# Performance work log

Measured on AMD Instinct MI355X. Metric: run time of the kernel, lower is better.

## Reference

```python
import jax, jax.numpy as jnp
import numpy as np

ALPHA = 0.2  # LeakyReLU negative slope
NEG_INF = -9e15


def setup_inputs() -> dict:
    key = jax.random.key(0)
    ks = jax.random.split(key, 6)
    N, IN, OUT, E = 2048, 256, 256, 64
    inp = {
        "input": jax.random.normal(ks[0], (N, IN), dtype=jnp.float32),
        "adj": jax.random.randint(ks[1], (N, N), 0, 2, dtype=jnp.int32),
        "e_feat": jax.random.normal(ks[2], (N, N, E), dtype=jnp.float32),
        # xavier-uniform-like scale for params
        "W_e": jax.random.normal(ks[3], (E, IN), dtype=jnp.float32) * (1.414 * np.sqrt(2.0 / (E + IN))),
        "W": jax.random.normal(ks[4], (IN, OUT), dtype=jnp.float32) * (1.414 * np.sqrt(2.0 / (IN + OUT))),
        "a": jax.random.normal(ks[5], (3 * OUT, 1), dtype=jnp.float32) * (1.414 * np.sqrt(2.0 / (3 * OUT + 1))),
    }
    return inp


def reference(input, adj, e_feat, W_e, W, a):
    F = W.shape[1]
    # Decompose attention vector: cat([h_i, h_j, e_ij]) @ a == h_i@a1 + h_j@a2 + e_ij@a3
    a1, a2, a3 = a[:F, 0], a[F:2 * F, 0], a[2 * F:, 0]
    h = input @ W                              # [N, F]
    s_src = h @ a1                             # [N]
    s_dst = h @ a2                             # [N]
    # e_ij @ a3 where e = e_feat @ W_e @ W, folded by associativity into one [N,N] result
    s_edge = e_feat @ (W_e @ (W @ a3))         # [N, N]
    scores = jax.nn.leaky_relu(s_src[:, None] + s_dst[None, :] + s_edge, negative_slope=ALPHA)
    att = jnp.where(adj > 0, scores, NEG_INF)
    att = jax.nn.softmax(att, axis=1)
    h_prime = att @ h                          # [N, F]
    return jax.nn.elu(h_prime)                 # concat=True -> ELU
```

## Files before the change

### kernel.cpp

```cpp
#include <hip/hip_runtime.h>
#include <math.h>

#define NN   2048
#define INF_ 256
#define OUTF 256
#define EF   64
#define ALPHA 0.2f
#define NEG_INF -9000000000000000.0f

typedef unsigned short ushortT;
typedef __attribute__((ext_vector_type(8))) short    short8v;
typedef __attribute__((ext_vector_type(4))) short    short4v;
typedef __attribute__((ext_vector_type(8))) unsigned short u16x8;
typedef __attribute__((ext_vector_type(4))) float    f32x4;
typedef __attribute__((ext_vector_type(4))) float    fv4;
typedef __attribute__((ext_vector_type(4))) int      iv4;

__device__ __forceinline__ ushortT f2b(float f) {
    unsigned b = *(unsigned*)&f;
    unsigned r = (b + 0x7FFFu + ((b >> 16) & 1u)) >> 16;
    return (ushortT)r;
}
__device__ __forceinline__ float dpp_add_xor1(float x) {
    int xi = *(int*)&x;
    int r = __builtin_amdgcn_mov_dpp(xi, 0xB1, 0xF, 0xF, true);
    float rf = *(float*)&r;
    return x + rf;
}
__device__ __forceinline__ float dpp_add_xor2(float x) {
    int xi = *(int*)&x;
    int r = __builtin_amdgcn_mov_dpp(xi, 0x4E, 0xF, 0xF, true);
    float rf = *(float*)&r;
    return x + rf;
}
__device__ __forceinline__ fv4 ntload4(const float* p) {
    return __builtin_nontemporal_load((const fv4*)p);
}

__global__ void prep1_kernel(const float* __restrict__ W, const float* __restrict__ a,
                             float* __restrict__ w3) {
    int lane = threadIdx.x & 63, wave = threadIdx.x >> 6;
    const float* a3 = a + 2 * OUTF;
    float4 av = *(const float4*)&a3[lane * 4];
    int r0 = blockIdx.x * 8 + wave * 2;
    #pragma unroll
    for (int rr = 0; rr < 2; ++rr) {
        int r = r0 + rr;
        float4 wv = *(const float4*)&W[(size_t)r * OUTF + lane * 4];
        float d = wv.x * av.x + wv.y * av.y + wv.z * av.z + wv.w * av.w;
        #pragma unroll
        for (int off = 32; off; off >>= 1) d += __shfl_xor(d, off);
        if (lane == 0) w3[r] = d;
    }
}

__global__ void prep2_kernel(const float* __restrict__ W_e, const float* __restrict__ w3,
                             float* __restrict__ we3) {
    int lane = threadIdx.x & 63, wave = threadIdx.x >> 6;
    int r = blockIdx.x * 4 + wave;
    float4 wv = *(const float4*)&W_e[(size_t)r * INF_ + lane * 4];
    float4 xv = *(const float4*)&w3[lane * 4];
    float d = wv.x * xv.x + wv.y * xv.y + wv.z * xv.z + wv.w * xv.w;
    #pragma unroll
    for (int off = 32; off; off >>= 1) d += __shfl_xor(d, off);
    if (lane == 0) we3[r] = d;
}

template<int K>
__launch_bounds__(256, 2)
__global__ void gemm_kernel(const float* __restrict__ A, const float* __restrict__ Bm,
                            float* __restrict__ C) {
    __shared__ float As[64][68];
    __shared__ float Bs[64][32];
    int tid = threadIdx.x;
    int r0 = blockIdx.x * 64;
    int c0 = blockIdx.y * 32;
    int tr = tid >> 4;
    int tc = tid & 15;
    float acc[4][2] = {};

    for (int k0 = 0; k0 < K; k0 += 64) {
        #pragma unroll
        for (int t = 0; t < 4; ++t) {
            int s = tid + t * 256;
            int row = s >> 4, col4 = s & 15;
            *(float4*)&As[row][col4 * 4] =
                *(const float4*)&A[(size_t)(r0 + row) * K + k0 + col4 * 4];
        }
        #pragma unroll
        for (int t = 0; t < 2; ++t) {
            int s = tid + t * 256;
            int row = s >> 3, col4 = s & 7;
            *(float4*)&Bs[row][col4 * 4] =
                *(const float4*)&Bm[(size_t)(k0 + row) * 256 + c0 + col4 * 4];
        }
        __syncthreads();
        #pragma unroll
        for (int kk = 0; kk < 64; kk += 4) {
            float4 aReg[4];
            float2 bReg[4];
            #pragma unroll
            for (int i = 0; i < 4; ++i) aReg[i] = *(const float4*)&As[tr * 4 + i][kk];
            #pragma unroll
            for (int q = 0; q < 4; ++q)  bReg[q] = *(const float2*)&Bs[kk + q][tc * 2];
            #pragma unroll
            for (int q = 0; q < 4; ++q) {
                float bx = bReg[q].x, by = bReg[q].y;
                #pragma unroll
                for (int i = 0; i < 4; ++i) {
                    float av = (q == 0) ? aReg[i].x : (q == 1) ? aReg[i].y
                             : (q == 2) ? aReg[i].z : aReg[i].w;
                    acc[i][0] += av * bx;
                    acc[i][1] += av * by;
                }
            }
        }
        __syncthreads();
    }
    #pragma unroll
    for (int i = 0; i < 4; ++i) {
        int r = r0 + tr * 4 + i;
        float2 v = {acc[i][0], acc[i][1]};
        *(float2*)&C[(size_t)r * 256 + c0 + tc * 2] = v;
    }
}

__global__ void xpose_sv_kernel(const float* __restrict__ h, const float* __restrict__ a,
                                ushortT* __restrict__ hbT,
                                float* __restrict__ s_src, float* __restrict__ s_dst) {
    __shared__ ushortT tb[64][72];
    int b = blockIdx.x;
    int t = threadIdx.x;
    if (b < 128) {
        int r0 = (b >> 2) * 64;
        int n0 = (b & 3) * 64;
        int row = t >> 2, seg = t & 3;
        #pragma unroll
        for (int c = 0; c < 4; ++c) {
            float4 v = *(const float4*)&h[(size_t)(r0 + row) * OUTF + n0 + seg * 16 + c * 4];
            tb[seg * 16 + c * 4 + 0][row] = f2b(v.x);
            tb[seg * 16 + c * 4 + 1][row] = f2b(v.y);
            tb[seg * 16 + c * 4 + 2][row] = f2b(v.z);
            tb[seg * 16 + c * 4 + 3][row] = f2b(v.w);
        }
        __syncthreads();
        *(u16x8*)&hbT[(size_t)(n0 + row) * NN + r0 + seg * 16] =
            *(const u16x8*)&tb[row][seg * 16];
        *(u16x8*)&hbT[(size_t)(n0 + row) * NN + r0 + seg * 16 + 8] =
            *(const u16x8*)&tb[row][seg * 16 + 8];
    } else {
        int lane = t & 63;
        int wave = t >> 6;
        int i = (b - 128) * 4 + wave;
        float acc1 = 0.f, acc2 = 0.f;
        #pragma unroll
        for (int u = 0; u < 4; ++u) {
            int o = lane + u * 64;
            float hv = h[(size_t)i * OUTF + o];
            acc1 += hv * a[o];
            acc2 += hv * a[OUTF + o];
        }
        #pragma unroll
        for (int off = 32; off; off >>= 1) {
            acc1 += __shfl_xor(acc1, off);
            acc2 += __shfl_xor(acc2, off);
        }
        if (lane == 0) { s_src[i] = acc1; s_dst[i] = acc2; }
    }
}

__launch_bounds__(256, 2)
__global__ void gemm2_mfma_kernel(const ushortT* __restrict__ attb,
                                  const ushortT* __restrict__ hbT,
                                  float* __restrict__ Cpart) {
    __shared__ ushortT As[64][72];
    __shared__ ushortT Bs[64][72];
    int tid = threadIdx.x;
    int lane = tid & 63;
    int w = tid >> 6;
    int r0 = blockIdx.x * 64;
    int c0 = blockIdx.y * 64;
    int z  = blockIdx.z;
    int m = lane & 15, q = lane >> 4;
    const int srow = tid >> 2, sseg = tid & 3;

    f32x4 acc0 = {0.f, 0.f, 0.f, 0.f};
    f32x4 acc1 = {0.f, 0.f, 0.f, 0.f};
    f32x4 acc2 = {0.f, 0.f, 0.f, 0.f};
    f32x4 acc3 = {0.f, 0.f, 0.f, 0.f};

    for (int k0 = z * (NN / 4); k0 < (z + 1) * (NN / 4); k0 += 64) {
        {
            const size_t abase = (size_t)(r0 + srow) * NN + k0 + sseg * 16;
            *(u16x8*)&As[srow][sseg * 16]     = *(const u16x8*)&attb[abase];
            *(u16x8*)&As[srow][sseg * 16 + 8] = *(const u16x8*)&attb[abase + 8];
            const size_t bbase = (size_t)(c0 + srow) * NN + k0 + sseg * 16;
            *(u16x8*)&Bs[srow][sseg * 16]     = *(const u16x8*)&hbT[bbase];
            *(u16x8*)&Bs[srow][sseg * 16 + 8] = *(const u16x8*)&hbT[bbase + 8];
        }
        __syncthreads();
        #pragma unroll
        for (int kk = 0; kk < 2; ++kk) {
            short4v a0 = *(const short4v*)&As[w * 16 + m][kk * 32 + q * 4];
            short4v a1 = *(const short4v*)&As[w * 16 + m][kk * 32 + 16 + q * 4];
            short8v af = {a0.x, a0.y, a0.z, a0.w, a1.x, a1.y, a1.z, a1.w};
            #pragma unroll
            for (int nb = 0; nb < 4; ++nb) {
                short4v b0 = *(const short4v*)&Bs[nb * 16 + m][kk * 32 + q * 4];
                short4v b1 = *(const short4v*)&Bs[nb * 16 + m][kk * 32 + 16 + q * 4];
                short8v bf = {b0.x, b0.y, b0.z, b0.w, b1.x, b1.y, b1.z, b1.w};
                if (nb == 0) acc0 = __builtin_amdgcn_mfma_f32_16x16x32_bf16(af, bf, acc0, 0, 0, 0);
                if (nb == 1) acc1 = __builtin_amdgcn_mfma_f32_16x16x32_bf16(af, bf, acc1, 0, 0, 0);
                if (nb == 2) acc2 = __builtin_amdgcn_mfma_f32_16x16x32_bf16(af, bf, acc2, 0, 0, 0);
                if (nb == 3) acc3 = __builtin_amdgcn_mfma_f32_16x16x32_bf16(af, bf, acc3, 0, 0, 0);
            }
        }
        __syncthreads();
    }
    float* Cz = Cpart + (size_t)z * NN * OUTF;
    #pragma unroll
    for (int r = 0; r < 4; ++r) {
        int row = r0 + w * 16 + q * 4 + r;
        Cz[(size_t)row * OUTF + c0 + 0  + m] = acc0[r];
        Cz[(size_t)row * OUTF + c0 + 16 + m] = acc1[r];
        Cz[(size_t)row * OUTF + c0 + 32 + m] = acc2[r];
        Cz[(size_t)row * OUTF + c0 + 48 + m] = acc3[r];
    }
}

__global__ void combine_kernel(const float* __restrict__ Cpart, const float* __restrict__ invs,
                               float* __restrict__ out) {
    int i = blockIdx.x, t = threadIdx.x;
    size_t idx = (size_t)i * OUTF + t;
    const size_t P = (size_t)NN * OUTF;
    float v = (Cpart[idx] + Cpart[P + idx] + Cpart[2 * P + idx] + Cpart[3 * P + idx]) * invs[i];
    out[idx] = v > 0.f ? v : __expf(v) - 1.f;
}

__launch_bounds__(256, 6)
__global__ void score_kernel(const float* __restrict__ e_feat, const int* __restrict__ adj,
                             const float* __restrict__ s_src, const float* __restrict__ s_dst,
                             const float* __restrict__ we3,
                             ushortT* __restrict__ attb, float* __restrict__ invs) {
    __shared__ float p[NN];
    __shared__ float sdst[NN];
    __shared__ unsigned char amask[NN];
    __shared__ float swe3[EF];
    __shared__ float redm[4], reds[4];

    int tid  = threadIdx.x;
    int lane = tid & 63;
    int wave = tid >> 6;
    int i    = blockIdx.x;

    const int* arow = adj + (size_t)i * NN;
    #pragma unroll
    for (int t = 0; t < 2; ++t) {
        int s = tid * 2 + t;
        iv4 a4 = __builtin_nontemporal_load(&((const iv4*)arow)[s]);
        uchar4 m4;
        m4.x = a4.x != 0; m4.y = a4.y != 0; m4.z = a4.z != 0; m4.w = a4.w != 0;
        *(uchar4*)&amask[s * 4] = m4;
        ((float4*)sdst)[s] = ((const float4*)s_dst)[s];
    }
    if (tid < EF) swe3[tid] = we3[tid];
    __syncthreads();

    const int g  = lane >> 2;
    const int gl = lane & 3;
    const float4 wv0 = *(const float4*)&swe3[0  + gl * 4];
    const float4 wv1 = *(const float4*)&swe3[16 + gl * 4];
    const float4 wv2 = *(const float4*)&swe3[32 + gl * 4];
    const float4 wv3 = *(const float4*)&swe3[48 + gl * 4];
    const float* efrow = e_feat + (size_t)i * NN * EF;
    const int joff = wave * 16 + g;

    unsigned mbits = 0;
    #pragma unroll
    for (int k = 0; k < 32; ++k)
        mbits |= (unsigned)(amask[k * 64 + joff] != 0) << k;

    #pragma unroll 4
    for (int k = 0; k < 32; ++k) {
        int j = k * 64 + joff;
        bool av = (mbits >> k) & 1u;
        fv4 e0, e1, e2, e3;
        if (av) {
            const float* ep = efrow + (size_t)j * EF;
            e0 = ntload4(&ep[0  + gl * 4]);
            e1 = ntload4(&ep[16 + gl * 4]);
            e2 = ntload4(&ep[32 + gl * 4]);
            e3 = ntload4(&ep[48 + gl * 4]);
        }
        if (av) {
            float d = e0.x * wv0.x + e0.y * wv0.y + e0.z * wv0.z + e0.w * wv0.w
                    + e1.x * wv1.x + e1.y * wv1.y + e1.z * wv1.z + e1.w * wv1.w
                    + e2.x * wv2.x + e2.y * wv2.y + e2.z * wv2.z + e2.w * wv2.w
                    + e3.x * wv3.x + e3.y * wv3.y + e3.z * wv3.z + e3.w * wv3.w;
            d = dpp_add_xor1(d);
            d = dpp_add_xor2(d);
            if (gl == 0) p[j] = d;
        }
    }
    __syncthreads();

    const float ssrc = s_src[i];

    float m = NEG_INF;
    for (int j = tid; j < NN; j += 256) {
        if (amask[j]) {
            float s = ssrc + sdst[j] + p[j];
            s = (s > 0.f) ? s : ALPHA * s;
            m = fmaxf(m, s);
        }
    }
    #pragma unroll
    for (int off = 32; off; off >>= 1) m = fmaxf(m, __shfl_xor(m, off));
    if (lane == 0) redm[wave] = m;
    __syncthreads();
    m = fmaxf(fmaxf(redm[0], redm[1]), fmaxf(redm[2], redm[3]));
    const bool none = (m < -8.0e14f);

    ushortT* arowo = attb + (size_t)i * NN;
    float sum = 0.f;
    for (int j = tid * 2; j < NN; j += 512) {
        float e0, e1;
        if (amask[j]) {
            float s = ssrc + sdst[j] + p[j];
            s = (s > 0.f) ? s : ALPHA * s;
            e0 = __expf(s - m);
        } else e0 = none ? 1.0f : 0.0f;
        if (amask[j + 1]) {
            float s = ssrc + sdst[j + 1] + p[j + 1];
            s = (s > 0.f) ? s : ALPHA * s;
            e1 = __expf(s - m);
        } else e1 = none ? 1.0f : 0.0f;
        ushort2 uu; uu.x = f2b(e0); uu.y = f2b(e1);
        *(ushort2*)&arowo[j] = uu;
        sum += e0 + e1;
    }
    #pragma unroll
    for (int off = 32; off; off >>= 1) sum += __shfl_xor(sum, off);
    if (lane == 0) reds[wave] = sum;
    __syncthreads();
    if (tid == 0) invs[i] = 1.f / (reds[0] + reds[1] + reds[2] + reds[3]);
}

extern "C" void kernel_launch(void* const* d_in, const int* in_sizes, int n_in,
                              void* d_out, int out_size, void* d_ws, size_t ws_size,
                              hipStream_t stream) {
    const float* input  = (const float*)d_in[0];
    const int*   adj    = (const int*)  d_in[1];
    const float* e_feat = (const float*)d_in[2];
    const float* W_e    = (const float*)d_in[3];
    const float* W      = (const float*)d_in[4];
    const float* a      = (const float*)d_in[5];
    float* out = (float*)d_out;

    float*   ws    = (float*)d_ws;
    float*   h     = ws;
    float*   s_src = h + (size_t)NN * OUTF;
    float*   s_dst = s_src + NN;
    float*   w3    = s_dst + NN;
    float*   we3   = w3 + INF_;
    float*   invs  = we3 + EF;
    ushortT* attb  = (ushortT*)(invs + NN);
    ushortT* hbT   = attb + (size_t)NN * NN;
    float*   cpart = (float*)(hbT + (size_t)OUTF * NN);

    prep1_kernel<<<32, 256, 0, stream>>>(W, a, w3);
    prep2_kernel<<<16, 256, 0, stream>>>(W_e, w3, we3);
    gemm_kernel<INF_><<<dim3(NN / 64, 8), 256, 0, stream>>>(input, W, h);
    xpose_sv_kernel<<<128 + NN / 4, 256, 0, stream>>>(h, a, hbT, s_src, s_dst);
    score_kernel<<<NN, 256, 0, stream>>>(e_feat, adj, s_src, s_dst, we3, attb, invs);
    gemm2_mfma_kernel<<<dim3(NN / 64, OUTF / 64, 4), 256, 0, stream>>>(attb, hbT, cpart);
    combine_kernel<<<NN, 256, 0, stream>>>(cpart, invs, out);
}
```

Baseline: 141.6 us.

## Fold attention vectors into W and merge h GEMM into score mega-kernel

```diff
diff --git a/kernel.cpp b/kernel.cpp
--- a/kernel.cpp
+++ b/kernel.cpp
@@ -37,128 +37,55 @@
     return __builtin_nontemporal_load((const fv4*)p);
 }
 
-__global__ void prep1_kernel(const float* __restrict__ W, const float* __restrict__ a,
-                             float* __restrict__ w3) {
+__global__ void prep_w_kernel(const float* __restrict__ W, const float* __restrict__ a,
+                              float* __restrict__ wa1, float* __restrict__ wa2,
+                              float* __restrict__ w3) {
     int lane = threadIdx.x & 63, wave = threadIdx.x >> 6;
-    const float* a3 = a + 2 * OUTF;
-    float4 av = *(const float4*)&a3[lane * 4];
+    float4 a1v = *(const float4*)&a[lane * 4];
+    float4 a2v = *(const float4*)&a[OUTF + lane * 4];
+    float4 a3v = *(const float4*)&a[2 * OUTF + lane * 4];
     int r0 = blockIdx.x * 8 + wave * 2;
     #pragma unroll
     for (int rr = 0; rr < 2; ++rr) {
         int r = r0 + rr;
         float4 wv = *(const float4*)&W[(size_t)r * OUTF + lane * 4];
-        float d = wv.x * av.x + wv.y * av.y + wv.z * av.z + wv.w * av.w;
+        float d1 = wv.x * a1v.x + wv.y * a1v.y + wv.z * a1v.z + wv.w * a1v.w;
+        float d2 = wv.x * a2v.x + wv.y * a2v.y + wv.z * a2v.z + wv.w * a2v.w;
+        float d3 = wv.x * a3v.x + wv.y * a3v.y + wv.z * a3v.z + wv.w * a3v.w;
+        #pragma unroll
+        for (int off = 32; off; off >>= 1) {
+            d1 += __shfl_xor(d1, off);
+            d2 += __shfl_xor(d2, off);
+            d3 += __shfl_xor(d3, off);
+        }
+        if (lane == 0) { wa1[r] = d1; wa2[r] = d2; w3[r] = d3; }
+    }
+}
+
+__global__ void prep2_sv2_kernel(const float* __restrict__ W_e, const float* __restrict__ w3,
+                                 const float* __restrict__ input,
+                                 const float* __restrict__ wa1, const float* __restrict__ wa2,
+                                 float* __restrict__ we3,
+                                 float* __restrict__ s_src, float* __restrict__ s_dst) {
+    int b = blockIdx.x, t = threadIdx.x;
+    int lane = t & 63, wave = t >> 6;
+    if (b < 16) {
+        int r = b * 4 + wave;
+        float4 wv = *(const float4*)&W_e[(size_t)r * INF_ + lane * 4];
+        float4 xv = *(const float4*)&w3[lane * 4];
+        float d = wv.x * xv.x + wv.y * xv.y + wv.z * xv.z + wv.w * xv.w;
         #pragma unroll
         for (int off = 32; off; off >>= 1) d += __shfl_xor(d, off);
-        if (lane == 0) w3[r] = d;
-    }
-}
-
-__global__ void prep2_kernel(const float* __restrict__ W_e, const float* __restrict__ w3,
-                             float* __restrict__ we3) {
-    int lane = threadIdx.x & 63, wave = threadIdx.x >> 6;
-    int r = blockIdx.x * 4 + wave;
-    float4 wv = *(const float4*)&W_e[(size_t)r * INF_ + lane * 4];
-    float4 xv = *(const float4*)&w3[lane * 4];
-    float d = wv.x * xv.x + wv.y * xv.y + wv.z * xv.z + wv.w * xv.w;
-    #pragma unroll
-    for (int off = 32; off; off >>= 1) d += __shfl_xor(d, off);
-    if (lane == 0) we3[r] = d;
-}
-
-template<int K>
-__launch_bounds__(256, 2)
-__global__ void gemm_kernel(const float* __restrict__ A, const float* __restrict__ Bm,
-                            float* __restrict__ C) {
-    __shared__ float As[64][68];
-    __shared__ float Bs[64][32];
-    int tid = threadIdx.x;
-    int r0 = blockIdx.x * 64;
-    int c0 = blockIdx.y * 32;
-    int tr = tid >> 4;
-    int tc = tid & 15;
-    float acc[4][2] = {};
-
-    for (int k0 = 0; k0 < K; k0 += 64) {
-        #pragma unroll
-        for (int t = 0; t < 4; ++t) {
-            int s = tid + t * 256;
-            int row = s >> 4, col4 = s & 15;
-            *(float4*)&As[row][col4 * 4] =
-                *(const float4*)&A[(size_t)(r0 + row) * K + k0 + col4 * 4];
-        }
-        #pragma unroll
-        for (int t = 0; t < 2; ++t) {
-            int s = tid + t * 256;
-            int row = s >> 3, col4 = s & 7;
-            *(float4*)&Bs[row][col4 * 4] =
-                *(const float4*)&Bm[(size_t)(k0 + row) * 256 + c0 + col4 * 4];
-        }
-        __syncthreads();
-        #pragma unroll
-        for (int kk = 0; kk < 64; kk += 4) {
-            float4 aReg[4];
-            float2 bReg[4];
-            #pragma unroll
-            for (int i = 0; i < 4; ++i) aReg[i] = *(const float4*)&As[tr * 4 + i][kk];
-            #pragma unroll
-            for (int q = 0; q < 4; ++q)  bReg[q] = *(const float2*)&Bs[kk + q][tc * 2];
-            #pragma unroll
-            for (int q = 0; q < 4; ++q) {
-                float bx = bReg[q].x, by = bReg[q].y;
-                #pragma unroll
-                for (int i = 0; i < 4; ++i) {
-                    float av = (q == 0) ? aReg[i].x : (q == 1) ? aReg[i].y
-                             : (q == 2) ? aReg[i].z : aReg[i].w;
-                    acc[i][0] += av * bx;
-                    acc[i][1] += av * by;
-                }
-            }
-        }
-        __syncthreads();
-    }
-    #pragma unroll
-    for (int i = 0; i < 4; ++i) {
-        int r = r0 + tr * 4 + i;
-        float2 v = {acc[i][0], acc[i][1]};
-        *(float2*)&C[(size_t)r * 256 + c0 + tc * 2] = v;
-    }
-}
-
-__global__ void xpose_sv_kernel(const float* __restrict__ h, const float* __restrict__ a,
-                                ushortT* __restrict__ hbT,
-                                float* __restrict__ s_src, float* __restrict__ s_dst) {
-    __shared__ ushortT tb[64][72];
-    int b = blockIdx.x;
-    int t = threadIdx.x;
-    if (b < 128) {
-        int r0 = (b >> 2) * 64;
-        int n0 = (b & 3) * 64;
-        int row = t >> 2, seg = t & 3;
-        #pragma unroll
-        for (int c = 0; c < 4; ++c) {
-            float4 v = *(const float4*)&h[(size_t)(r0 + row) * OUTF + n0 + seg * 16 + c * 4];
-            tb[seg * 16 + c * 4 + 0][row] = f2b(v.x);
-            tb[seg * 16 + c * 4 + 1][row] = f2b(v.y);
-            tb[seg * 16 + c * 4 + 2][row] = f2b(v.z);
-            tb[seg * 16 + c * 4 + 3][row] = f2b(v.w);
-        }
-        __syncthreads();
-        *(u16x8*)&hbT[(size_t)(n0 + row) * NN + r0 + seg * 16] =
-            *(const u16x8*)&tb[row][seg * 16];
-        *(u16x8*)&hbT[(size_t)(n0 + row) * NN + r0 + seg * 16 + 8] =
-            *(const u16x8*)&tb[row][seg * 16 + 8];
+        if (lane == 0) we3[r] = d;
     } else {
-        int lane = t & 63;
-        int wave = t >> 6;
-        int i = (b - 128) * 4 + wave;
+        int i = (b - 16) * 4 + wave;
         float acc1 = 0.f, acc2 = 0.f;
         #pragma unroll
         for (int u = 0; u < 4; ++u) {
             int o = lane + u * 64;
-            float hv = h[(size_t)i * OUTF + o];
-            acc1 += hv * a[o];
-            acc2 += hv * a[OUTF + o];
+            float iv = input[(size_t)i * INF_ + o];
+            acc1 += iv * wa1[o];
+            acc2 += iv * wa2[o];
         }
         #pragma unroll
         for (int off = 32; off; off >>= 1) {
@@ -169,89 +96,98 @@
     }
 }
 
-__launch_bounds__(256, 2)
-__global__ void gemm2_mfma_kernel(const ushortT* __restrict__ attb,
-                                  const ushortT* __restrict__ hbT,
-                                  float* __restrict__ Cpart) {
-    __shared__ ushortT As[64][72];
-    __shared__ ushortT Bs[64][72];
+struct ScSmem {
+    float p[NN];
+    float sdst[NN];
+    unsigned char amask[NN];
+    float swe3[EF];
+    float redm[4], reds[4];
+};
+struct GmSmem {
+    float As[64][68];
+    float Bs[64][32];
+};
+union MegaSmem { ScSmem sc; GmSmem gm; };
+
+__launch_bounds__(256, 6)
+__global__ void mega_kernel(const float* __restrict__ input, const float* __restrict__ W,
+                            const float* __restrict__ e_feat, const int* __restrict__ adj,
+                            const float* __restrict__ s_src, const float* __restrict__ s_dst,
+                            const float* __restrict__ we3,
+                            ushortT* __restrict__ hbT, ushortT* __restrict__ attb,
+                            float* __restrict__ invs) {
+    __shared__ MegaSmem smem;
+    int b   = blockIdx.x;
     int tid = threadIdx.x;
     int lane = tid & 63;
-    int w = tid >> 6;
-    int r0 = blockIdx.x * 64;
-    int c0 = blockIdx.y * 64;
-    int z  = blockIdx.z;
-    int m = lane & 15, q = lane >> 4;
-    const int srow = tid >> 2, sseg = tid & 3;
-
-    f32x4 acc0 = {0.f, 0.f, 0.f, 0.f};
-    f32x4 acc1 = {0.f, 0.f, 0.f, 0.f};
-    f32x4 acc2 = {0.f, 0.f, 0.f, 0.f};
-    f32x4 acc3 = {0.f, 0.f, 0.f, 0.f};
-
-    for (int k0 = z * (NN / 4); k0 < (z + 1) * (NN / 4); k0 += 64) {
-        {
-            const size_t abase = (size_t)(r0 + srow) * NN + k0 + sseg * 16;
-            *(u16x8*)&As[srow][sseg * 16]     = *(const u16x8*)&attb[abase];
-            *(u16x8*)&As[srow][sseg * 16 + 8] = *(const u16x8*)&attb[abase + 8];
-            const size_t bbase = (size_t)(c0 + srow) * NN + k0 + sseg * 16;
-            *(u16x8*)&Bs[srow][sseg * 16]     = *(const u16x8*)&hbT[bbase];
-            *(u16x8*)&Bs[srow][sseg * 16 + 8] = *(const u16x8*)&hbT[bbase + 8];
+    int wave = tid >> 6;
+
+    if (b < 256) {
+        int r0 = (b >> 3) * 64;
+        int c0 = (b & 7) * 32;
+        int tr = tid >> 4;
+        int tc = tid & 15;
+        float acc[4][2] = {};
+
+        for (int k0 = 0; k0 < INF_; k0 += 64) {
+            #pragma unroll
+            for (int t = 0; t < 4; ++t) {
+                int s = tid + t * 256;
+                int row = s >> 4, col4 = s & 15;
+                *(float4*)&smem.gm.As[row][col4 * 4] =
+                    *(const float4*)&input[(size_t)(r0 + row) * INF_ + k0 + col4 * 4];
+            }
+            #pragma unroll
+            for (int t = 0; t < 2; ++t) {
+                int s = tid + t * 256;
+                int row = s >> 3, col4 = s & 7;
+                *(float4*)&smem.gm.Bs[row][col4 * 4] =
+                    *(const float4*)&W[(size_t)(k0 + row) * 256 + c0 + col4 * 4];
+            }
+            __syncthreads();
+            #pragma unroll
+            for (int kk = 0; kk < 64; kk += 4) {
+                float4 aReg[4];
+                float2 bReg[4];
+                #pragma unroll
+                for (int i = 0; i < 4; ++i) aReg[i] = *(const float4*)&smem.gm.As[tr * 4 + i][kk];
+                #pragma unroll
+                for (int q = 0; q < 4; ++q)  bReg[q] = *(const float2*)&smem.gm.Bs[kk + q][tc * 2];
+                #pragma unroll
+                for (int q = 0; q < 4; ++q) {
+                    float bx = bReg[q].x, by = bReg[q].y;
+                    #pragma unroll
+                    for (int i = 0; i < 4; ++i) {
+                        float av = (q == 0) ? aReg[i].x : (q == 1) ? aReg[i].y
+                                 : (q == 2) ? aReg[i].z : aReg[i].w;
+                        acc[i][0] += av * bx;
+                        acc[i][1] += av * by;
+                    }
+                }
+            }
+            __syncthreads();
+        }
+        ushortT (*tb)[72] = (ushortT (*)[72])smem.gm.Bs;
+        #pragma unroll
+        for (int i = 0; i < 4; ++i) {
+            int row = tr * 4 + i;
+            tb[tc * 2 + 0][row] = f2b(acc[i][0]);
+            tb[tc * 2 + 1][row] = f2b(acc[i][1]);
         }
         __syncthreads();
-        #pragma unroll
-        for (int kk = 0; kk < 2; ++kk) {
-            short4v a0 = *(const short4v*)&As[w * 16 + m][kk * 32 + q * 4];
-            short4v a1 = *(const short4v*)&As[w * 16 + m][kk * 32 + 16 + q * 4];
-            short8v af = {a0.x, a0.y, a0.z, a0.w, a1.x, a1.y, a1.z, a1.w};
-            #pragma unroll
-            for (int nb = 0; nb < 4; ++nb) {
-                short4v b0 = *(const short4v*)&Bs[nb * 16 + m][kk * 32 + q * 4];
-                short4v b1 = *(const short4v*)&Bs[nb * 16 + m][kk * 32 + 16 + q * 4];
-                short8v bf = {b0.x, b0.y, b0.z, b0.w, b1.x, b1.y, b1.z, b1.w};
-                if (nb == 0) acc0 = __builtin_amdgcn_mfma_f32_16x16x32_bf16(af, bf, acc0, 0, 0, 0);
-                if (nb == 1) acc1 = __builtin_amdgcn_mfma_f32_16x16x32_bf16(af, bf, acc1, 0, 0, 0);
-                if (nb == 2) acc2 = __builtin_amdgcn_mfma_f32_16x16x32_bf16(af, bf, acc2, 0, 0, 0);
-                if (nb == 3) acc3 = __builtin_amdgcn_mfma_f32_16x16x32_bf16(af, bf, acc3, 0, 0, 0);
-            }
-        }
-        __syncthreads();
-    }
-    float* Cz = Cpart + (size_t)z * NN * OUTF;
-    #pragma unroll
-    for (int r = 0; r < 4; ++r) {
-        int row = r0 + w * 16 + q * 4 + r;
-        Cz[(size_t)row * OUTF + c0 + 0  + m] = acc0[r];
-        Cz[(size_t)row * OUTF + c0 + 16 + m] = acc1[r];
-        Cz[(size_t)row * OUTF + c0 + 32 + m] = acc2[r];
-        Cz[(size_t)row * OUTF + c0 + 48 + m] = acc3[r];
-    }
-}
-
-__global__ void combine_kernel(const float* __restrict__ Cpart, const float* __restrict__ invs,
-                               float* __restrict__ out) {
-    int i = blockIdx.x, t = threadIdx.x;
-    size_t idx = (size_t)i * OUTF + t;
-    const size_t P = (size_t)NN * OUTF;
-    float v = (Cpart[idx] + Cpart[P + idx] + Cpart[2 * P + idx] + Cpart[3 * P + idx]) * invs[i];
-    out[idx] = v > 0.f ? v : __expf(v) - 1.f;
-}
-
-__launch_bounds__(256, 6)
-__global__ void score_kernel(const float* __restrict__ e_feat, const int* __restrict__ adj,
-                             const float* __restrict__ s_src, const float* __restrict__ s_dst,
-                             const float* __restrict__ we3,
-                             ushortT* __restrict__ attb, float* __restrict__ invs) {
-    __shared__ float p[NN];
-    __shared__ float sdst[NN];
-    __shared__ unsigned char amask[NN];
-    __shared__ float swe3[EF];
-    __shared__ float redm[4], reds[4];
-
-    int tid  = threadIdx.x;
-    int lane = tid & 63;
-    int wave = tid >> 6;
-    int i    = blockIdx.x;
+        int n = tid >> 3, seg = tid & 7;
+        *(u16x8*)&hbT[(size_t)(c0 + n) * NN + r0 + seg * 8] =
+            *(const u16x8*)&tb[n][seg * 8];
+        return;
+    }
+
+    int i = b - 256;
+    float* p    = smem.sc.p;
+    float* sdst = smem.sc.sdst;
+    unsigned char* amask = smem.sc.amask;
+    float* swe3 = smem.sc.swe3;
+    float* redm = smem.sc.redm;
+    float* reds = smem.sc.reds;
 
     const int* arow = adj + (size_t)i * NN;
     #pragma unroll
@@ -346,6 +282,74 @@
     if (tid == 0) invs[i] = 1.f / (reds[0] + reds[1] + reds[2] + reds[3]);
 }
 
+__launch_bounds__(256, 2)
+__global__ void gemm2_mfma_kernel(const ushortT* __restrict__ attb,
+                                  const ushortT* __restrict__ hbT,
+                                  float* __restrict__ Cpart) {
+    __shared__ ushortT As[64][72];
+    __shared__ ushortT Bs[64][72];
+    int tid = threadIdx.x;
+    int lane = tid & 63;
+    int w = tid >> 6;
+    int r0 = blockIdx.x * 64;
+    int c0 = blockIdx.y * 64;
+    int z  = blockIdx.z;
+    int m = lane & 15, q = lane >> 4;
+    const int srow = tid >> 2, sseg = tid & 3;
+
+    f32x4 acc0 = {0.f, 0.f, 0.f, 0.f};
+    f32x4 acc1 = {0.f, 0.f, 0.f, 0.f};
+    f32x4 acc2 = {0.f, 0.f, 0.f, 0.f};
+    f32x4 acc3 = {0.f, 0.f, 0.f, 0.f};
+
+    for (int k0 = z * (NN / 4); k0 < (z + 1) * (NN / 4); k0 += 64) {
+        {
+            const size_t abase = (size_t)(r0 + srow) * NN + k0 + sseg * 16;
+            *(u16x8*)&As[srow][sseg * 16]     = *(const u16x8*)&attb[abase];
+            *(u16x8*)&As[srow][sseg * 16 + 8] = *(const u16x8*)&attb[abase + 8];
+            const size_t bbase = (size_t)(c0 + srow) * NN + k0 + sseg * 16;
+            *(u16x8*)&Bs[srow][sseg * 16]     = *(const u16x8*)&hbT[bbase];
+            *(u16x8*)&Bs[srow][sseg * 16 + 8] = *(const u16x8*)&hbT[bbase + 8];
+        }
+        __syncthreads();
+        #pragma unroll
+        for (int kk = 0; kk < 2; ++kk) {
+            short4v a0 = *(const short4v*)&As[w * 16 + m][kk * 32 + q * 4];
+            short4v a1 = *(const short4v*)&As[w * 16 + m][kk * 32 + 16 + q * 4];
+            short8v af = {a0.x, a0.y, a0.z, a0.w, a1.x, a1.y, a1.z, a1.w};
+            #pragma unroll
+            for (int nb = 0; nb < 4; ++nb) {
+                short4v b0 = *(const short4v*)&Bs[nb * 16 + m][kk * 32 + q * 4];
+                short4v b1 = *(const short4v*)&Bs[nb * 16 + m][kk * 32 + 16 + q * 4];
+                short8v bf = {b0.x, b0.y, b0.z, b0.w, b1.x, b1.y, b1.z, b1.w};
+                if (nb == 0) acc0 = __builtin_amdgcn_mfma_f32_16x16x32_bf16(af, bf, acc0, 0, 0, 0);
+                if (nb == 1) acc1 = __builtin_amdgcn_mfma_f32_16x16x32_bf16(af, bf, acc1, 0, 0, 0);
+                if (nb == 2) acc2 = __builtin_amdgcn_mfma_f32_16x16x32_bf16(af, bf, acc2, 0, 0, 0);
+                if (nb == 3) acc3 = __builtin_amdgcn_mfma_f32_16x16x32_bf16(af, bf, acc3, 0, 0, 0);
+            }
+        }
+        __syncthreads();
+    }
+    float* Cz = Cpart + (size_t)z * NN * OUTF;
+    #pragma unroll
+    for (int r = 0; r < 4; ++r) {
+        int row = r0 + w * 16 + q * 4 + r;
+        Cz[(size_t)row * OUTF + c0 + 0  + m] = acc0[r];
+        Cz[(size_t)row * OUTF + c0 + 16 + m] = acc1[r];
+        Cz[(size_t)row * OUTF + c0 + 32 + m] = acc2[r];
+        Cz[(size_t)row * OUTF + c0 + 48 + m] = acc3[r];
+    }
+}
+
+__global__ void combine_kernel(const float* __restrict__ Cpart, const float* __restrict__ invs,
+                               float* __restrict__ out) {
+    int i = blockIdx.x, t = threadIdx.x;
+    size_t idx = (size_t)i * OUTF + t;
+    const size_t P = (size_t)NN * OUTF;
+    float v = (Cpart[idx] + Cpart[P + idx] + Cpart[2 * P + idx] + Cpart[3 * P + idx]) * invs[i];
+    out[idx] = v > 0.f ? v : __expf(v) - 1.f;
+}
+
 extern "C" void kernel_launch(void* const* d_in, const int* in_sizes, int n_in,
                               void* d_out, int out_size, void* d_ws, size_t ws_size,
                               hipStream_t stream) {
@@ -358,21 +362,22 @@
     float* out = (float*)d_out;
 
     float*   ws    = (float*)d_ws;
-    float*   h     = ws;
-    float*   s_src = h + (size_t)NN * OUTF;
+    float*   wa1   = ws;
+    float*   wa2   = wa1 + INF_;
+    float*   w3    = wa2 + INF_;
+    float*   we3   = w3 + INF_;
+    float*   s_src = we3 + EF;
     float*   s_dst = s_src + NN;
-    float*   w3    = s_dst + NN;
-    float*   we3   = w3 + INF_;
-    float*   invs  = we3 + EF;
+    float*   invs  = s_dst + NN;
     ushortT* attb  = (ushortT*)(invs + NN);
     ushortT* hbT   = attb + (size_t)NN * NN;
     float*   cpart = (float*)(hbT + (size_t)OUTF * NN);
 
-    prep1_kernel<<<32, 256, 0, stream>>>(W, a, w3);
-    prep2_kernel<<<16, 256, 0, stream>>>(W_e, w3, we3);
-    gemm_kernel<INF_><<<dim3(NN / 64, 8), 256, 0, stream>>>(input, W, h);
-    xpose_sv_kernel<<<128 + NN / 4, 256, 0, stream>>>(h, a, hbT, s_src, s_dst);
-    score_kernel<<<NN, 256, 0, stream>>>(e_feat, adj, s_src, s_dst, we3, attb, invs);
+    prep_w_kernel<<<32, 256, 0, stream>>>(W, a, wa1, wa2, w3);
+    prep2_sv2_kernel<<<16 + NN / 4, 256, 0, stream>>>(W_e, w3, input, wa1, wa2,
+                                                      we3, s_src, s_dst);
+    mega_kernel<<<256 + NN, 256, 0, stream>>>(input, W, e_feat, adj, s_src, s_dst, we3,
+                                              hbT, attb, invs);
     gemm2_mfma_kernel<<<dim3(NN / 64, OUTF / 64, 4), 256, 0, stream>>>(attb, hbT, cpart);
     combine_kernel<<<NN, 256, 0, stream>>>(cpart, invs, out);
 }
```

New measurement: 184.5 us. 30.3% more time.
